# Performance work log

Hardware: AMD Instinct MI355X
Metric: run time of the kernel (lower is better)

The kernel has to match this reference:

```python
import jax, jax.numpy as jnp
import numpy as np

N_NODES = 100000
N_EDGES = 640000
N_LABEL = 100000
IN_C, HID_C, OUT_C = 128, 128, 64


def setup_inputs() -> dict:
    key = jax.random.key(0)
    ks = jax.random.split(key, 9)
    x = jax.random.normal(ks[0], (N_NODES, IN_C), dtype=jnp.float32)
    edge_index = jax.random.randint(ks[1], (2, N_EDGES), 0, N_NODES, dtype=jnp.int64)
    edge_label_index = jax.random.randint(ks[2], (2, N_LABEL), 0, N_NODES, dtype=jnp.int64)
    s = 0.05  # small init scale
    # PyG SAGEConv: lin_l applied to mean-aggregated neighbors (with bias), lin_r to root (no bias)
    W1l = jax.random.normal(ks[3], (HID_C, IN_C), dtype=jnp.float32) * s
    b1 = jnp.zeros((HID_C,), dtype=jnp.float32)
    W1r = jax.random.normal(ks[4], (HID_C, IN_C), dtype=jnp.float32) * s
    W2l = jax.random.normal(ks[5], (OUT_C, HID_C), dtype=jnp.float32) * s
    b2 = jnp.zeros((OUT_C,), dtype=jnp.float32)
    W2r = jax.random.normal(ks[6], (OUT_C, HID_C), dtype=jnp.float32) * s
    return {"x": x, "edge_index": edge_index, "edge_label_index": edge_label_index,
            "W1l": W1l, "b1": b1, "W1r": W1r, "W2l": W2l, "b2": b2, "W2r": W2r}


def _sage_conv(x, src, dst, Wl, b, Wr):
    # mean aggregation of source features at destination nodes
    agg = jax.ops.segment_sum(x[src], dst, num_segments=N_NODES)  # [N, d]
    cnt = jax.ops.segment_sum(jnp.ones((src.shape[0],), x.dtype), dst, num_segments=N_NODES)
    mean = agg / jnp.maximum(cnt, 1.0)[:, None]
    return mean @ Wl.T + b + x @ Wr.T


def reference(x, edge_index, edge_label_index, W1l, b1, W1r, W2l, b2, W2r):
    src, dst = edge_index[0], edge_index[1]
    h = jax.nn.relu(_sage_conv(x, src, dst, W1l, b1, W1r))
    z = _sage_conv(h, src, dst, W2l, b2, W2r)
    # edge-wise dot-product decode
    scores = jnp.sum(z[edge_label_index[0]] * z[edge_label_index[1]], axis=-1)  # [E_label]
    return scores
```

## Files before the change

kernel.cpp:

```cpp
#include <hip/hip_runtime.h>

#define N_NODES 100000
#define N_EDGES 640000
#define N_LABEL 100000
#define CAP 32

typedef __bf16 bf16x8 __attribute__((ext_vector_type(8)));
typedef float f32x4 __attribute__((ext_vector_type(4)));

#define CW1L 0
#define CB1  16384
#define CW1R 16512
#define CW2L 32896
#define CB2  41088
#define CW2R 41152
#define NWTS 49344

#define NB_W 193
#define NB_X 12500

__device__ __forceinline__ float bf2f(unsigned short u) {
    union { unsigned int i; float f; } c; c.i = ((unsigned int)u) << 16; return c.f;
}
__device__ __forceinline__ float asf(unsigned int u) {
    union { unsigned int i; float f; } c; c.i = u; return c.f;
}
__device__ __forceinline__ unsigned short f2bf(float f) {
    union { float f; unsigned int i; } c; c.f = f;
    unsigned int lsb = (c.i >> 16) & 1u;
    c.i += 0x7fffu + lsb;
    return (unsigned short)(c.i >> 16);
}

__global__ void k_detect(const unsigned int* __restrict__ xw,
                         const unsigned int* __restrict__ eiw,
                         int* __restrict__ flags) {
    int l = threadIdx.x;
    unsigned int w = xw[l];
    unsigned short lo = (unsigned short)(w & 0xffffu);
    int e = (lo >> 7) & 0xff;
    bool bf_like = (lo == 0) || (e >= 98 && e <= 138);
    unsigned long long m = __ballot(bf_like);
    unsigned int ew = eiw[2 * l + 1];
    unsigned long long mz = __ballot(ew == 0u);
    if (l == 0) {
        flags[0] = (__popcll(m) < 48) ? 1 : 0;
        flags[1] = (__popcll(mz) == 64) ? 1 : 0;
    }
}

__global__ void k_convwx(const void* W1l, const void* b1, const void* W1r,
                         const void* W2l, const void* b2, const void* W2r,
                         unsigned short* __restrict__ wts,
                         const void* __restrict__ x, unsigned short* __restrict__ xb,
                         const int* __restrict__ flags) {
    int b = blockIdx.x;
    int f32m = flags[0];
    if (b < NB_W) {
        int i = b * 256 + threadIdx.x;
        if (i >= NWTS) return;
        const void* src; int local;
        if      (i < CB1)  { src = W1l; local = i; }
        else if (i < CW1R) { src = b1;  local = i - CB1; }
        else if (i < CW2L) { src = W1r; local = i - CW1R; }
        else if (i < CB2)  { src = W2l; local = i - CW2L; }
        else if (i < CW2R) { src = b2;  local = i - CB2; }
        else               { src = W2r; local = i - CW2R; }
        wts[i] = f32m ? f2bf(((const float*)src)[local]) : ((const unsigned short*)src)[local];
    } else {
        int i = (b - NB_W) * 256 + threadIdx.x;
        if (i >= N_NODES * 32) return;
        if (f32m) {
            float4 p = ((const float4*)x)[i];
            ushort4 o;
            o.x = f2bf(p.x); o.y = f2bf(p.y); o.z = f2bf(p.z); o.w = f2bf(p.w);
            ((ushort4*)xb)[i] = o;
        } else {
            ((ushort4*)xb)[i] = ((const ushort4*)x)[i];
        }
    }
}

__global__ void k_fill(const int* __restrict__ ei, int* __restrict__ cnt,
                       int* __restrict__ csr, const int* __restrict__ flags) {
    int e = blockIdx.x * blockDim.x + threadIdx.x;
    if (e >= N_EDGES) return;
    int i64 = flags[1];
    int src = ei[e << i64], dst = ei[(N_EDGES + e) << i64];
    int pos = atomicAdd(&cnt[dst], 1);
    if (pos < CAP) csr[dst * CAP + pos] = src;
}

__global__ __launch_bounds__(256) void k_fused1(
    const int* __restrict__ cnt, const int* __restrict__ csr,
    const unsigned short* __restrict__ xb, const unsigned short* __restrict__ wts,
    unsigned short* __restrict__ tb)
{
    __shared__ unsigned short sm[32][136];
    int wave = threadIdx.x >> 6, lane = threadIdx.x & 63;
    int nb0 = blockIdx.x * 32;

    {
        int nA = nb0 + wave * 8;
        int half = lane >> 5, sl = lane & 31;
        int rows[4];
#pragma unroll
        for (int p = 0; p < 4; ++p)
            rows[p] = csr[(size_t)(nA + p * 2 + half) * CAP + sl];
        int dpre = (lane < 8) ? cnt[nA + lane] : 0;
        int c2 = lane << 1;

#pragma unroll
        for (int j = 0; j < 8; ++j) {
            int deg = __shfl(dpre, j);
            int m = deg < CAP ? deg : CAP;
            float s0 = 0.f, s1 = 0.f;
            for (int e0 = 0; e0 < m; e0 += 8) {
                unsigned int v[8];
#pragma unroll
                for (int u = 0; u < 8; ++u) {
                    int e = e0 + u;
                    int sidx = __shfl(rows[j >> 1], (j & 1) * 32 + e);
                    sidx = (e < m) ? sidx : 0;
                    v[u] = *(const unsigned int*)(xb + (size_t)sidx * 128 + c2);
                }
#pragma unroll
                for (int u = 0; u < 8; ++u) {
                    unsigned int w = ((e0 + u) < m) ? v[u] : 0u;
                    s0 += asf(w << 16);
                    s1 += asf(w & 0xffff0000u);
                }
            }
            float inv = 1.0f / (deg > 1 ? (float)deg : 1.0f);
            unsigned int o = (unsigned int)f2bf(s0 * inv) | ((unsigned int)f2bf(s1 * inv) << 16);
            *(unsigned int*)&sm[wave * 8 + j][c2] = o;
        }
    }
    __syncthreads();

    int qq = wave;
    int row = lane & 15, kq = lane >> 4;
    int col = lane & 15, rq = lane >> 4;
    f32x4 acc[2][2];
    {
        bf16x8 Wf[16];
#pragma unroll
        for (int t = 0; t < 2; ++t)
#pragma unroll
            for (int ks = 0; ks < 8; ++ks) {
                const int k0 = ks * 32;
                const unsigned short* base = wts + (k0 < 128 ? CW1L : CW1R)
                    + (size_t)(qq * 32 + t * 16 + row) * 128 + (k0 & 127) + kq * 8;
                Wf[t * 8 + ks] = *reinterpret_cast<const bf16x8*>(base);
            }
#pragma unroll
        for (int i = 0; i < 2; ++i) {
            bf16x8 Af[8];
#pragma unroll
            for (int ks = 0; ks < 4; ++ks)
                Af[ks] = *reinterpret_cast<const bf16x8*>(&sm[i * 16 + row][ks * 32 + kq * 8]);
            const unsigned short* rx = xb + (size_t)(nb0 + i * 16 + row) * 128 + kq * 8;
#pragma unroll
            for (int ks = 0; ks < 4; ++ks)
                Af[4 + ks] = *reinterpret_cast<const bf16x8*>(rx + ks * 32);
            acc[i][0] = (f32x4){0.f, 0.f, 0.f, 0.f};
            acc[i][1] = (f32x4){0.f, 0.f, 0.f, 0.f};
#pragma unroll
            for (int ks = 0; ks < 8; ++ks) {
                acc[i][0] = __builtin_amdgcn_mfma_f32_16x16x32_bf16(Af[ks], Wf[ks],     acc[i][0], 0, 0, 0);
                acc[i][1] = __builtin_amdgcn_mfma_f32_16x16x32_bf16(Af[ks], Wf[8 + ks], acc[i][1], 0, 0, 0);
            }
        }
    }
    __syncthreads();
    {
        float bias0 = bf2f(wts[CB1 + qq * 32 + col]);
        float bias1 = bf2f(wts[CB1 + qq * 32 + 16 + col]);
#pragma unroll
        for (int i = 0; i < 2; ++i)
#pragma unroll
            for (int r = 0; r < 4; ++r) {
                int nl = i * 16 + rq * 4 + r;
                float v0 = acc[i][0][r] + bias0; v0 = v0 > 0.f ? v0 : 0.f;
                float v1 = acc[i][1][r] + bias1; v1 = v1 > 0.f ? v1 : 0.f;
                sm[nl][qq * 32 + col]      = f2bf(v0);
                sm[nl][qq * 32 + 16 + col] = f2bf(v1);
            }
    }
    __syncthreads();

    {
        const size_t wbase = (qq < 2) ? (CW2L + (size_t)(qq * 32) * 128)
                                      : (CW2R + (size_t)((qq - 2) * 32) * 128);
        bf16x8 Wg[8];
#pragma unroll
        for (int t = 0; t < 2; ++t)
#pragma unroll
            for (int ks = 0; ks < 4; ++ks)
                Wg[t * 4 + ks] = *reinterpret_cast<const bf16x8*>(
                    wts + wbase + (size_t)(t * 16 + row) * 128 + ks * 32 + kq * 8);
#pragma unroll
        for (int i = 0; i < 2; ++i) {
            bf16x8 Ag[4];
#pragma unroll
            for (int ks = 0; ks < 4; ++ks)
                Ag[ks] = *reinterpret_cast<const bf16x8*>(&sm[i * 16 + row][ks * 32 + kq * 8]);
            f32x4 c0 = (f32x4){0.f, 0.f, 0.f, 0.f};
            f32x4 c1 = (f32x4){0.f, 0.f, 0.f, 0.f};
#pragma unroll
            for (int ks = 0; ks < 4; ++ks) {
                c0 = __builtin_amdgcn_mfma_f32_16x16x32_bf16(Ag[ks], Wg[ks],     c0, 0, 0, 0);
                c1 = __builtin_amdgcn_mfma_f32_16x16x32_bf16(Ag[ks], Wg[4 + ks], c1, 0, 0, 0);
            }
#pragma unroll
            for (int r = 0; r < 4; ++r) {
                int n = nb0 + i * 16 + rq * 4 + r;
                tb[(size_t)n * 128 + qq * 32 + col]      = f2bf(c0[r]);
                tb[(size_t)n * 128 + qq * 32 + 16 + col] = f2bf(c1[r]);
            }
        }
    }
}

__global__ __launch_bounds__(256) void k_agg2c(
    const int* __restrict__ cnt, const int* __restrict__ csr,
    const unsigned short* __restrict__ tb, const unsigned short* __restrict__ wts,
    unsigned short* __restrict__ zb) {
    int wv = (int)((blockIdx.x * blockDim.x + threadIdx.x) >> 6);
    int n2 = wv * 2;
    if (n2 >= N_NODES) return;
    int lane = threadIdx.x & 63;
    int half = lane >> 5, sl = lane & 31;
    int n = n2 + half;
    int dpre = (lane < 2) ? cnt[n2 + lane] : 0;
    int deg = __shfl(dpre, half);
    int m = deg < CAP ? deg : CAP;
    int mo = __shfl(m, lane ^ 32);
    int mmax = m > mo ? m : mo;
    int srcrow = csr[(size_t)n * CAP + sl];
    int c2 = sl << 1;
    float s0 = 0.f, s1 = 0.f;
    for (int e0 = 0; e0 < mmax; e0 += 8) {
        unsigned int v[8];
#pragma unroll
        for (int u = 0; u < 8; ++u) {
            int e = e0 + u;
            int sidx = __shfl(srcrow, half * 32 + e);
            sidx = (e < m) ? sidx : 0;
            v[u] = *(const unsigned int*)(tb + (size_t)sidx * 128 + c2);
        }
#pragma unroll
        for (int u = 0; u < 8; ++u) {
            unsigned int w = ((e0 + u) < m) ? v[u] : 0u;
            s0 += asf(w << 16);
            s1 += asf(w & 0xffff0000u);
        }
    }
    float inv = 1.0f / (deg > 1 ? (float)deg : 1.0f);
    unsigned int tr = *(const unsigned int*)(tb + (size_t)n * 128 + 64 + c2);
    unsigned int bb = *(const unsigned int*)(wts + CB2 + c2);
    float zx = s0 * inv + asf(bb << 16)          + asf(tr << 16);
    float zy = s1 * inv + asf(bb & 0xffff0000u)  + asf(tr & 0xffff0000u);
    unsigned int o = (unsigned int)f2bf(zx) | ((unsigned int)f2bf(zy) << 16);
    *(unsigned int*)(zb + (size_t)n * 64 + c2) = o;
}

__global__ void k_decode(const int* __restrict__ eli, const unsigned short* __restrict__ zb,
                         void* __restrict__ out, const int* __restrict__ flags) {
    long long t = (long long)blockIdx.x * blockDim.x + threadIdx.x;
    int e = (int)(t >> 3);
    if (e >= N_LABEL) return;
    int f32m = flags[0], i64 = flags[1];
    int q = threadIdx.x & 7;
    int a = eli[e << i64], b = eli[(N_LABEL + e) << i64];
    uint4 pa = *(const uint4*)(zb + (size_t)a * 64 + q * 8);
    uint4 pb = *(const uint4*)(zb + (size_t)b * 64 + q * 8);
    float s = asf(pa.x << 16) * asf(pb.x << 16) + asf(pa.x & 0xffff0000u) * asf(pb.x & 0xffff0000u)
            + asf(pa.y << 16) * asf(pb.y << 16) + asf(pa.y & 0xffff0000u) * asf(pb.y & 0xffff0000u)
            + asf(pa.z << 16) * asf(pb.z << 16) + asf(pa.z & 0xffff0000u) * asf(pb.z & 0xffff0000u)
            + asf(pa.w << 16) * asf(pb.w << 16) + asf(pa.w & 0xffff0000u) * asf(pb.w & 0xffff0000u);
#pragma unroll
    for (int off = 1; off < 8; off <<= 1) s += __shfl_xor(s, off);
    if (q == 0) {
        if (f32m) ((float*)out)[e] = s;
        else      ((unsigned short*)out)[e] = f2bf(s);
    }
}

extern "C" void kernel_launch(void* const* d_in, const int* in_sizes, int n_in,
                              void* d_out, int out_size, void* d_ws, size_t ws_size,
                              hipStream_t stream) {
    const void* x   = d_in[0];
    const int*  ei  = (const int*)d_in[1];
    const int*  eli = (const int*)d_in[2];
    const void* W1l = d_in[3];
    const void* b1  = d_in[4];
    const void* W1r = d_in[5];
    const void* W2l = d_in[6];
    const void* b2  = d_in[7];
    const void* W2r = d_in[8];

    char* ws = (char*)d_ws;
    const size_t offFlag = 0;
    const size_t offCnt  = 1024;
    const size_t offWts  = 801024;
    const size_t offCsr  = 1u << 20;
    const size_t offXb   = offCsr + (size_t)N_NODES * CAP * 4;
    const size_t offTb   = offXb  + (size_t)N_NODES * 128 * 2;
    const size_t offZb   = offTb  + (size_t)N_NODES * 128 * 2;

    int*            flags = (int*)(ws + offFlag);
    int*            cnt   = (int*)(ws + offCnt);
    unsigned short* wts   = (unsigned short*)(ws + offWts);
    int*            csr   = (int*)(ws + offCsr);
    unsigned short* xb    = (unsigned short*)(ws + offXb);
    unsigned short* tb    = (unsigned short*)(ws + offTb);
    unsigned short* zb    = (unsigned short*)(ws + offZb);

    hipMemsetAsync(ws, 0, 1u << 20, stream);

    k_detect<<<1, 64, 0, stream>>>((const unsigned int*)x, (const unsigned int*)ei, flags);

    k_convwx<<<NB_W + NB_X, 256, 0, stream>>>(W1l, b1, W1r, W2l, b2, W2r, wts, x, xb, flags);

    k_fill<<<(N_EDGES + 255) / 256, 256, 0, stream>>>(ei, cnt, csr, flags);

    k_fused1<<<N_NODES / 32, 256, 0, stream>>>(cnt, csr, xb, wts, tb);

    k_agg2c<<<12500, 256, 0, stream>>>(cnt, csr, tb, wts, zb);

    k_decode<<<(N_LABEL * 8) / 256, 256, 0, stream>>>(eli, zb, d_out, flags);
}
```

Before: 232.7 us.

## Split layer-2 transform buffer, fold memset into init kernel, double conversion work

Splits the layer-2 transformed features into two contiguous 64-wide arrays (neighbor part and root part), so the gather in the second aggregation reads dense 128-byte rows instead of half of 256-byte rows. The hipMemsetAsync and the detect kernel are merged into a single init kernel that zeroes the degree counts and sets the format flags, removing one launch. The x conversion blocks now each handle two chunks, which halves the grid. The gather layout change should improve cache-line utilisation, and the other two changes trim launch and scheduling overhead.

```diff
diff --git a/kernel.cpp b/kernel.cpp
--- a/kernel.cpp
+++ b/kernel.cpp
@@ -17,7 +17,7 @@
 #define NWTS 49344
 
 #define NB_W 193
-#define NB_X 12500
+#define NB_X 6250
 
 __device__ __forceinline__ float bf2f(unsigned short u) {
     union { unsigned int i; float f; } c; c.i = ((unsigned int)u) << 16; return c.f;
@@ -32,20 +32,24 @@
     return (unsigned short)(c.i >> 16);
 }
 
-__global__ void k_detect(const unsigned int* __restrict__ xw,
-                         const unsigned int* __restrict__ eiw,
-                         int* __restrict__ flags) {
-    int l = threadIdx.x;
-    unsigned int w = xw[l];
-    unsigned short lo = (unsigned short)(w & 0xffffu);
-    int e = (lo >> 7) & 0xff;
-    bool bf_like = (lo == 0) || (e >= 98 && e <= 138);
-    unsigned long long m = __ballot(bf_like);
-    unsigned int ew = eiw[2 * l + 1];
-    unsigned long long mz = __ballot(ew == 0u);
-    if (l == 0) {
-        flags[0] = (__popcll(m) < 48) ? 1 : 0;
-        flags[1] = (__popcll(mz) == 64) ? 1 : 0;
+__global__ void k_init(const unsigned int* __restrict__ xw,
+                       const unsigned int* __restrict__ eiw,
+                       int* __restrict__ flags, int* __restrict__ cnt) {
+    int i = blockIdx.x * blockDim.x + threadIdx.x;
+    if (i < N_NODES) cnt[i] = 0;
+    if (blockIdx.x == 0 && threadIdx.x < 64) {
+        int l = threadIdx.x;
+        unsigned int w = xw[l];
+        unsigned short lo = (unsigned short)(w & 0xffffu);
+        int e = (lo >> 7) & 0xff;
+        bool bf_like = (lo == 0) || (e >= 98 && e <= 138);
+        unsigned long long m = __ballot(bf_like);
+        unsigned int ew = eiw[2 * l + 1];
+        unsigned long long mz = __ballot(ew == 0u);
+        if (l == 0) {
+            flags[0] = (__popcll(m) < 48) ? 1 : 0;
+            flags[1] = (__popcll(mz) == 64) ? 1 : 0;
+        }
     }
 }
 
@@ -68,15 +72,19 @@
         else               { src = W2r; local = i - CW2R; }
         wts[i] = f32m ? f2bf(((const float*)src)[local]) : ((const unsigned short*)src)[local];
     } else {
-        int i = (b - NB_W) * 256 + threadIdx.x;
-        if (i >= N_NODES * 32) return;
-        if (f32m) {
-            float4 p = ((const float4*)x)[i];
-            ushort4 o;
-            o.x = f2bf(p.x); o.y = f2bf(p.y); o.z = f2bf(p.z); o.w = f2bf(p.w);
-            ((ushort4*)xb)[i] = o;
-        } else {
-            ((ushort4*)xb)[i] = ((const ushort4*)x)[i];
+        int base = (b - NB_W) * 512 + threadIdx.x;
+#pragma unroll
+        for (int g = 0; g < 2; ++g) {
+            int i = base + g * 256;
+            if (i >= N_NODES * 32) continue;
+            if (f32m) {
+                float4 p = ((const float4*)x)[i];
+                ushort4 o;
+                o.x = f2bf(p.x); o.y = f2bf(p.y); o.z = f2bf(p.z); o.w = f2bf(p.w);
+                ((ushort4*)xb)[i] = o;
+            } else {
+                ((ushort4*)xb)[i] = ((const ushort4*)x)[i];
+            }
         }
     }
 }
@@ -94,7 +102,7 @@
 __global__ __launch_bounds__(256) void k_fused1(
     const int* __restrict__ cnt, const int* __restrict__ csr,
     const unsigned short* __restrict__ xb, const unsigned short* __restrict__ wts,
-    unsigned short* __restrict__ tb)
+    unsigned short* __restrict__ tbl, unsigned short* __restrict__ tbr)
 {
     __shared__ unsigned short sm[32][136];
     int wave = threadIdx.x >> 6, lane = threadIdx.x & 63;
@@ -199,6 +207,8 @@
             for (int ks = 0; ks < 4; ++ks)
                 Wg[t * 4 + ks] = *reinterpret_cast<const bf16x8*>(
                     wts + wbase + (size_t)(t * 16 + row) * 128 + ks * 32 + kq * 8);
+        unsigned short* dst = (qq < 2) ? tbl : tbr;
+        int cb = (qq & 1) * 32;
 #pragma unroll
         for (int i = 0; i < 2; ++i) {
             bf16x8 Ag[4];
@@ -215,8 +225,8 @@
 #pragma unroll
             for (int r = 0; r < 4; ++r) {
                 int n = nb0 + i * 16 + rq * 4 + r;
-                tb[(size_t)n * 128 + qq * 32 + col]      = f2bf(c0[r]);
-                tb[(size_t)n * 128 + qq * 32 + 16 + col] = f2bf(c1[r]);
+                dst[(size_t)n * 64 + cb + col]      = f2bf(c0[r]);
+                dst[(size_t)n * 64 + cb + 16 + col] = f2bf(c1[r]);
             }
         }
     }
@@ -224,8 +234,8 @@
 
 __global__ __launch_bounds__(256) void k_agg2c(
     const int* __restrict__ cnt, const int* __restrict__ csr,
-    const unsigned short* __restrict__ tb, const unsigned short* __restrict__ wts,
-    unsigned short* __restrict__ zb) {
+    const unsigned short* __restrict__ tbl, const unsigned short* __restrict__ tbr,
+    const unsigned short* __restrict__ wts, unsigned short* __restrict__ zb) {
     int wv = (int)((blockIdx.x * blockDim.x + threadIdx.x) >> 6);
     int n2 = wv * 2;
     if (n2 >= N_NODES) return;
@@ -247,7 +257,7 @@
             int e = e0 + u;
             int sidx = __shfl(srcrow, half * 32 + e);
             sidx = (e < m) ? sidx : 0;
-            v[u] = *(const unsigned int*)(tb + (size_t)sidx * 128 + c2);
+            v[u] = *(const unsigned int*)(tbl + (size_t)sidx * 64 + c2);
         }
 #pragma unroll
         for (int u = 0; u < 8; ++u) {
@@ -257,7 +267,7 @@
         }
     }
     float inv = 1.0f / (deg > 1 ? (float)deg : 1.0f);
-    unsigned int tr = *(const unsigned int*)(tb + (size_t)n * 128 + 64 + c2);
+    unsigned int tr = *(const unsigned int*)(tbr + (size_t)n * 64 + c2);
     unsigned int bb = *(const unsigned int*)(wts + CB2 + c2);
     float zx = s0 * inv + asf(bb << 16)          + asf(tr << 16);
     float zy = s1 * inv + asf(bb & 0xffff0000u)  + asf(tr & 0xffff0000u);
@@ -306,28 +316,29 @@
     const size_t offWts  = 801024;
     const size_t offCsr  = 1u << 20;
     const size_t offXb   = offCsr + (size_t)N_NODES * CAP * 4;
-    const size_t offTb   = offXb  + (size_t)N_NODES * 128 * 2;
-    const size_t offZb   = offTb  + (size_t)N_NODES * 128 * 2;
+    const size_t offTbl  = offXb  + (size_t)N_NODES * 128 * 2;
+    const size_t offTbr  = offTbl + (size_t)N_NODES * 64 * 2;
+    const size_t offZb   = offTbr + (size_t)N_NODES * 64 * 2;
 
     int*            flags = (int*)(ws + offFlag);
     int*            cnt   = (int*)(ws + offCnt);
     unsigned short* wts   = (unsigned short*)(ws + offWts);
     int*            csr   = (int*)(ws + offCsr);
     unsigned short* xb    = (unsigned short*)(ws + offXb);
-    unsigned short* tb    = (unsigned short*)(ws + offTb);
+    unsigned short* tbl   = (unsigned short*)(ws + offTbl);
+    unsigned short* tbr   = (unsigned short*)(ws + offTbr);
     unsigned short* zb    = (unsigned short*)(ws + offZb);
 
-    hipMemsetAsync(ws, 0, 1u << 20, stream);
-
-    k_detect<<<1, 64, 0, stream>>>((const unsigned int*)x, (const unsigned int*)ei, flags);
+    k_init<<<(N_NODES + 255) / 256, 256, 0, stream>>>((const unsigned int*)x,
+                                                      (const unsigned int*)ei, flags, cnt);
 
     k_convwx<<<NB_W + NB_X, 256, 0, stream>>>(W1l, b1, W1r, W2l, b2, W2r, wts, x, xb, flags);
 
     k_fill<<<(N_EDGES + 255) / 256, 256, 0, stream>>>(ei, cnt, csr, flags);
 
-    k_fused1<<<N_NODES / 32, 256, 0, stream>>>(cnt, csr, xb, wts, tb);
-
-    k_agg2c<<<12500, 256, 0, stream>>>(cnt, csr, tb, wts, zb);
+    k_fused1<<<N_NODES / 32, 256, 0, stream>>>(cnt, csr, xb, wts, tbl, tbr);
+
+    k_agg2c<<<12500, 256, 0, stream>>>(cnt, csr, tbl, tbr, wts, zb);
 
     k_decode<<<(N_LABEL * 8) / 256, 256, 0, stream>>>(eli, zb, d_out, flags);
 }
```

New measurement: 232.6 us. No clear change (-0.0%).
